# Optimization experiments

Measured on AMD Instinct MI355X. Metric: run time of the kernel, lower is better.

Reference implementation:

```python
import jax, jax.numpy as jnp
import numpy as np

N = 20000      # nodes
E = 200000     # edges
IN = 128       # in_feat
OUT = 128      # out_feat
NB = 8         # num_bases
SI = IN // NB  # submat_in = 16
SO = OUT // NB # submat_out = 16
R = 230        # num_rels
T = 365        # total_times


def setup_inputs() -> dict:
    key = jax.random.key(0)
    ks = jax.random.split(key, 11)
    h = jax.random.normal(ks[0], (N, IN), jnp.float32)
    edge_norm = jax.random.uniform(ks[1], (E, 1), jnp.float32)
    node_norm = jax.random.uniform(ks[2], (N, 1), jnp.float32)
    weight = jax.random.normal(ks[3], (R, NB * SI * SO), jnp.float32) * 0.05
    h_bias = jnp.zeros((OUT,), jnp.float32)
    loop_weight = jax.random.normal(ks[4], (IN, OUT), jnp.float32) * 0.05
    time_embed = jax.random.normal(ks[5], (T, IN), jnp.float32) * 0.05
    edge_src = jax.random.randint(ks[6], (E,), 0, N)
    edge_dst = jax.random.randint(ks[7], (E,), 0, N)
    edge_type = jax.random.randint(ks[8], (E,), 0, R)
    time_idx = jax.random.randint(ks[9], (N,), 0, T)
    return dict(h=h, edge_norm=edge_norm, node_norm=node_norm, weight=weight,
                h_bias=h_bias, loop_weight=loop_weight, time_embed=time_embed,
                edge_src=edge_src, edge_dst=edge_dst, edge_type=edge_type,
                time_idx=time_idx)


def reference(h, edge_norm, node_norm, weight, h_bias, loop_weight, time_embed,
              edge_src, edge_dst, edge_type, time_idx):
    # self-loop message
    loop_message = h @ loop_weight                              # [N, OUT]
    # msg_func: per-edge relation weight gather + block-diagonal bmm
    W_e = weight[edge_type].reshape(-1, NB, SI, SO)             # [E, NB, SI, SO]
    src = h[edge_src].reshape(-1, NB, SI)                       # [E, NB, SI]
    msg = jnp.einsum('ebi,ebio->ebo', src, W_e).reshape(-1, OUT)  # [E, OUT]
    msg = msg * edge_norm
    # fn.sum aggregation over destination nodes
    agg = jax.ops.segment_sum(msg, edge_dst, num_segments=N)    # [N, OUT]
    # apply_func: scale by node norm, then bias + self loop + activation
    node_repr = agg * node_norm
    node_repr = node_repr + h_bias + loop_message
    node_repr = jax.nn.relu(node_repr)
    # get_time_embedding: per-node time embedding gather
    time_embedding = time_embed[time_idx]                       # [N, IN]
    return node_repr, time_embedding
```

## Files before the change

### kernel.cpp

```cpp
#include <hip/hip_runtime.h>
#include <hip/hip_bf16.h>

#define N 20000
#define E 200000
#define IN 128
#define OUT 128
#define NB 8
#define SI 16
#define SO 16
#define R 230
#define T 365

__device__ float g_agg[(size_t)N * OUT];

__global__ void zero_agg_kernel() {
    long i = (long)blockIdx.x * blockDim.x + threadIdx.x;
    long stride = (long)gridDim.x * blockDim.x;
    for (; i < (long)N * OUT; i += stride) g_agg[i] = 0.f;
}

__global__ void edge_kernel(const float* __restrict__ h,
                            const float* __restrict__ edge_norm,
                            const float* __restrict__ weight,
                            const int* __restrict__ edge_src,
                            const int* __restrict__ edge_dst,
                            const int* __restrict__ edge_type) {
    long idx = (long)blockIdx.x * blockDim.x + threadIdx.x;
    int e = (int)(idx >> 7);
    if (e >= E) return;
    int o  = (int)(idx & 127);
    int b  = o >> 4;
    int ol = o & 15;
    int s = edge_src[e];
    int d = edge_dst[e];
    int r = edge_type[e];
    const float* src = h + (long)s * IN + b * SI;
    const float* W   = weight + (long)r * (NB * SI * SO) + b * (SI * SO) + ol;
    float acc = 0.f;
#pragma unroll
    for (int i = 0; i < SI; ++i)
        acc = fmaf(src[i], W[i * SO], acc);
    acc *= edge_norm[e];
    atomicAdd(&g_agg[(long)d * OUT + o], acc);
}

__global__ __launch_bounds__(128) void node_kernel(
        const float* __restrict__ h,
        const float* __restrict__ node_norm,
        const float* __restrict__ h_bias,
        const float* __restrict__ loop_weight,
        const float* __restrict__ time_embed,
        const int* __restrict__ time_idx,
        float* __restrict__ out) {
    __shared__ float hsm[IN * 16];
    const int tid  = threadIdx.x;
    const int base = blockIdx.x * 16;

    for (int k = tid; k < 16 * IN; k += 128) {
        int nl = k >> 7;
        int i  = k & 127;
        hsm[i * 16 + nl] = h[(long)(base + nl) * IN + i];
    }
    __syncthreads();

    float acc[16];
#pragma unroll
    for (int nl = 0; nl < 16; ++nl) acc[nl] = 0.f;

    for (int i = 0; i < IN; ++i) {
        float w = loop_weight[(long)i * OUT + tid];
        const float4* hp = reinterpret_cast<const float4*>(&hsm[i * 16]);
#pragma unroll
        for (int q = 0; q < 4; ++q) {
            float4 hv = hp[q];
            acc[q * 4 + 0] = fmaf(hv.x, w, acc[q * 4 + 0]);
            acc[q * 4 + 1] = fmaf(hv.y, w, acc[q * 4 + 1]);
            acc[q * 4 + 2] = fmaf(hv.z, w, acc[q * 4 + 2]);
            acc[q * 4 + 3] = fmaf(hv.w, w, acc[q * 4 + 3]);
        }
    }

    float bias = h_bias[tid];
#pragma unroll
    for (int nl = 0; nl < 16; ++nl) {
        int n = base + nl;
        float v = g_agg[(long)n * OUT + tid] * node_norm[n] + bias + acc[nl];
        out[(long)n * OUT + tid] = fmaxf(v, 0.f);
        out[(long)N * OUT + (long)n * IN + tid] =
            time_embed[(long)time_idx[n] * IN + tid];
    }
}

extern "C" void kernel_launch(void* const* d_in, const int* in_sizes, int n_in,
                              void* d_out, int out_size, void* d_ws, size_t ws_size,
                              hipStream_t stream) {
    const float* h           = (const float*)d_in[0];
    const float* edge_norm   = (const float*)d_in[1];
    const float* node_norm   = (const float*)d_in[2];
    const float* weight      = (const float*)d_in[3];
    const float* h_bias      = (const float*)d_in[4];
    const float* loop_weight = (const float*)d_in[5];
    const float* time_embed  = (const float*)d_in[6];
    const int*   edge_src    = (const int*)d_in[7];
    const int*   edge_dst    = (const int*)d_in[8];
    const int*   edge_type   = (const int*)d_in[9];
    const int*   time_idx    = (const int*)d_in[10];
    float* out = (float*)d_out;

    zero_agg_kernel<<<2560, 256, 0, stream>>>();

    const long total = (long)E * 128;
    const int  bs = 256;
    edge_kernel<<<(int)((total + bs - 1) / bs), bs, 0, stream>>>(
        h, edge_norm, weight, edge_src, edge_dst, edge_type);

    node_kernel<<<N / 16, 128, 0, stream>>>(
        h, node_norm, h_bias, loop_weight, time_embed, time_idx, out);
}
```

Baseline: 240.0 us.

## Replace atomic scatter aggregation with CSR sort-by-destination pull aggregation

Builds a CSR grouping of edges by destination (count, single-block scan, atomic scatter) and transposes the relation weights so each output row is contiguous. Each node then pulls its incoming edges in a per-node block and writes its aggregate directly, with no float atomics and no zeroing pass. In exchange it adds several small kernels, including a single-block scan, and the order of edges within a node's segment, and so the summation order, is nondeterministic. Per-node work is also imbalanced across nodes of different degree.

Result: slower. 297.1 us (+23.8%).

```diff
diff --git a/kernel.cpp b/kernel.cpp
--- a/kernel.cpp
+++ b/kernel.cpp
@@ -12,36 +12,108 @@
 #define T 365
 
 __device__ float g_agg[(size_t)N * OUT];
+__device__ int   g_deg[N];
+__device__ int   g_off[N + 1];
+__device__ int   g_cur[N];
+__device__ int   g_srt_src[E];
+__device__ int   g_srt_typ[E];
+__device__ float g_srt_nrm[E];
+__device__ float g_wt[(size_t)R * NB * SI * SO];
 
-__global__ void zero_agg_kernel() {
-    long i = (long)blockIdx.x * blockDim.x + threadIdx.x;
-    long stride = (long)gridDim.x * blockDim.x;
-    for (; i < (long)N * OUT; i += stride) g_agg[i] = 0.f;
+__global__ void zero_deg_kernel() {
+    int i = blockIdx.x * blockDim.x + threadIdx.x;
+    if (i < N) g_deg[i] = 0;
 }
 
-__global__ void edge_kernel(const float* __restrict__ h,
-                            const float* __restrict__ edge_norm,
-                            const float* __restrict__ weight,
-                            const int* __restrict__ edge_src,
-                            const int* __restrict__ edge_dst,
-                            const int* __restrict__ edge_type) {
-    long idx = (long)blockIdx.x * blockDim.x + threadIdx.x;
-    int e = (int)(idx >> 7);
+__global__ void transpose_w_kernel(const float* __restrict__ weight) {
+    int k = blockIdx.x * blockDim.x + threadIdx.x;
+    if (k >= R * NB * SI * SO) return;
+    int r    = k >> 11;
+    int rem  = k & 2047;
+    int b    = rem >> 8;
+    int rem2 = rem & 255;
+    int i    = rem2 >> 4;
+    int ol   = rem2 & 15;
+    g_wt[(long)r * 2048 + b * 256 + ol * 16 + i] = weight[k];
+}
+
+__global__ void count_kernel(const int* __restrict__ edge_dst) {
+    int e = blockIdx.x * blockDim.x + threadIdx.x;
+    if (e < E) atomicAdd(&g_deg[edge_dst[e]], 1);
+}
+
+__global__ __launch_bounds__(1024) void scan_kernel() {
+    __shared__ int part[1024];
+    const int t = threadIdx.x;
+    const int base = t * 20;
+    int csum = 0;
+    int d[20];
+#pragma unroll
+    for (int k = 0; k < 20; ++k) {
+        int idx = base + k;
+        d[k] = (idx < N) ? g_deg[idx] : 0;
+        csum += d[k];
+    }
+    part[t] = csum;
+    __syncthreads();
+    for (int off = 1; off < 1024; off <<= 1) {
+        int v = (t >= off) ? part[t - off] : 0;
+        __syncthreads();
+        part[t] += v;
+        __syncthreads();
+    }
+    int run = part[t] - csum;
+#pragma unroll
+    for (int k = 0; k < 20; ++k) {
+        int idx = base + k;
+        if (idx < N) {
+            g_off[idx] = run;
+            g_cur[idx] = run;
+            run += d[k];
+        }
+    }
+    if (t == 1023) g_off[N] = part[1023];
+}
+
+__global__ void scatter_kernel(const int* __restrict__ edge_src,
+                               const int* __restrict__ edge_dst,
+                               const int* __restrict__ edge_type,
+                               const float* __restrict__ edge_norm) {
+    int e = blockIdx.x * blockDim.x + threadIdx.x;
     if (e >= E) return;
-    int o  = (int)(idx & 127);
-    int b  = o >> 4;
-    int ol = o & 15;
-    int s = edge_src[e];
-    int d = edge_dst[e];
-    int r = edge_type[e];
-    const float* src = h + (long)s * IN + b * SI;
-    const float* W   = weight + (long)r * (NB * SI * SO) + b * (SI * SO) + ol;
+    int dnode = edge_dst[e];
+    int pos = atomicAdd(&g_cur[dnode], 1);
+    g_srt_src[pos] = edge_src[e];
+    g_srt_typ[pos] = edge_type[e];
+    g_srt_nrm[pos] = edge_norm[e];
+}
+
+__global__ __launch_bounds__(128) void agg_kernel(const float* __restrict__ h) {
+    const int n   = blockIdx.x;
+    const int tid = threadIdx.x;
+    const int b   = tid >> 4;
+    const int ol  = tid & 15;
+    const int j0 = g_off[n], j1 = g_off[n + 1];
     float acc = 0.f;
+    for (int j = j0; j < j1; ++j) {
+        int   s  = g_srt_src[j];
+        int   r  = g_srt_typ[j];
+        float nr = g_srt_nrm[j];
+        const float4* hp = reinterpret_cast<const float4*>(h + (long)s * IN + b * SI);
+        const float4* wp = reinterpret_cast<const float4*>(g_wt + (long)r * 2048 + b * 256 + ol * SI);
+        float dot = 0.f;
 #pragma unroll
-    for (int i = 0; i < SI; ++i)
-        acc = fmaf(src[i], W[i * SO], acc);
-    acc *= edge_norm[e];
-    atomicAdd(&g_agg[(long)d * OUT + o], acc);
+        for (int q = 0; q < 4; ++q) {
+            float4 a = hp[q];
+            float4 w = wp[q];
+            dot = fmaf(a.x, w.x, dot);
+            dot = fmaf(a.y, w.y, dot);
+            dot = fmaf(a.z, w.z, dot);
+            dot = fmaf(a.w, w.w, dot);
+        }
+        acc = fmaf(dot, nr, acc);
+    }
+    g_agg[(long)n * OUT + tid] = acc;
 }
 
 __global__ __launch_bounds__(128) void node_kernel(
@@ -107,13 +179,13 @@
     const int*   time_idx    = (const int*)d_in[10];
     float* out = (float*)d_out;
 
-    zero_agg_kernel<<<2560, 256, 0, stream>>>();
-
-    const long total = (long)E * 128;
-    const int  bs = 256;
-    edge_kernel<<<(int)((total + bs - 1) / bs), bs, 0, stream>>>(
-        h, edge_norm, weight, edge_src, edge_dst, edge_type);
-
+    zero_deg_kernel<<<(N + 255) / 256, 256, 0, stream>>>();
+    transpose_w_kernel<<<(R * NB * SI * SO + 255) / 256, 256, 0, stream>>>(weight);
+    count_kernel<<<(E + 255) / 256, 256, 0, stream>>>(edge_dst);
+    scan_kernel<<<1, 1024, 0, stream>>>();
+    scatter_kernel<<<(E + 255) / 256, 256, 0, stream>>>(
+        edge_src, edge_dst, edge_type, edge_norm);
+    agg_kernel<<<N, 128, 0, stream>>>(h);
     node_kernel<<<N / 16, 128, 0, stream>>>(
         h, node_norm, h_bias, loop_weight, time_embed, time_idx, out);
 }
```
